# Kernel tuning notes

Measured on AMD Instinct MI355X. Metric: run time of the kernel, lower is better.

Reference implementation:

```python
import jax, jax.numpy as jnp
import numpy as np


def _weighted_sample(key, w, n_draw):
    # Inverse-CDF weighted sampling with replacement; prob proportional to relu(w).
    # Matches torch.multinomial over the strictly-positive (top-cnt sorted) entries,
    # since zero-weight columns are never selected with side='right'.
    cdf = jnp.cumsum(jnp.maximum(w, 0.0), axis=1)                     # [R, C]
    u = jax.random.uniform(key, (w.shape[0], n_draw), dtype=w.dtype) * cdf[:, -1:]
    idx = jax.vmap(lambda c, q: jnp.searchsorted(c, q, side='right'))(cdf, u)
    return jax.lax.stop_gradient(jnp.minimum(idx, w.shape[1] - 1))    # [R, K] column ids


def contrast_loss(key, padj, nadj, px, nx):
    R, Cp = padj.shape
    Cn = nadj.shape[1]
    K = min(Cp, Cn)  # num = min(pcnt, ncnt) <= K always
    pcnt = jnp.sum(padj > 0, axis=1)
    ncnt = jnp.sum(nadj > 0, axis=1)
    num = jnp.minimum(pcnt, ncnt)                                     # [R] int
    pinc = jnp.argsort(padj, axis=1)                                  # ascending, like torch.sort
    ninc = jnp.argsort(nadj, axis=1)
    kp, kn = jax.random.split(key)
    samp_n = _weighted_sample(kn, nadj, K)                            # sampled negative cols
    samp_p = _weighted_sample(kp, padj, K)                            # sampled positive cols
    j = jnp.arange(K)
    mask = (j[None, :] < num[:, None]).astype(px.dtype)               # first num draws count
    rows = jnp.arange(R)[:, None]
    # top-num entries of the ascending sort: positions C-num .. C-1
    top_p = jnp.clip(Cp - num[:, None] + j[None, :], 0, Cp - 1)
    top_n = jnp.clip(Cn - num[:, None] + j[None, :], 0, Cn - 1)
    pos_A = jnp.take_along_axis(pinc, top_p, axis=1)                  # branch num==pcnt
    neg_B = jnp.take_along_axis(ninc, top_n, axis=1)                  # branch num==ncnt<pcnt
    termA = jnp.maximum(nx[rows, samp_n] - px[rows, pos_A] + 1.0, 0.0)
    termB = jnp.maximum(nx[rows, neg_B] - px[rows, samp_p] + 1.0, 0.0)
    branchA = (pcnt <= ncnt)[:, None]                                 # num == pcnt
    term = jnp.where(branchA, termA, termB) * mask
    row_loss = term.sum(axis=1) / jnp.maximum(num, 1).astype(px.dtype)
    return jnp.where(num > 0, row_loss, 0.0).sum()


def _forward(KUU_adj, VUU_adj, Vuser, Vitem, Kuser, Kitem, preference, Vpreference, structure):
    key = jax.random.key(42)
    k0, k1, k2, k3 = jax.random.split(key, 4)
    f32 = VUU_adj.dtype
    # --- Vu: V-user vs V-user ---
    Vu_adj = Vuser @ Vuser.T                                          # [Nv, Nv]
    n = Vu_adj.shape[0]
    tmp1 = 1.0 - (VUU_adj > 0).astype(f32) - jnp.eye(n, dtype=f32)
    Vu = contrast_loss(k0, VUU_adj, tmp1, Vu_adj, Vu_adj)
    # --- Ku: K-user vs K-user (last 3 cols are negatives) ---
    Ku_adj = Kuser @ Kuser.T                                          # [Nk, Nk]
    Kc = KUU_adj.shape[1]
    tmp2 = (1.0 - (KUU_adj > 0).astype(f32) - jnp.eye(Kc, dtype=f32))[:n, -3:]
    Ku = contrast_loss(k1, KUU_adj[:n, :Kc - 3], tmp2,
                       Ku_adj[:n, :Kc - 3], Ku_adj[:n, -3:])
    # --- Vi: V-user vs V-item (binarization of tmp3 is overwritten in the original) ---
    Vi_adj = Vuser @ Vitem.T                                          # [Nv, NvI]
    VUI_adj = Vpreference.T
    Vi = contrast_loss(k2, VUI_adj, 1.0 - VUI_adj, Vi_adj, Vi_adj)
    # --- Ki: first 5 K-users vs K-item ---
    Ki_adj = Kuser[:5, :] @ Kitem.T                                   # [5, NkI]
    KUI_adj = preference.T
    Ki = contrast_loss(k3, KUI_adj, 1.0 - KUI_adj, Ki_adj, Ki_adj)
    # --- ii: item-item structure alignment ---
    ii_adj = Kitem @ Vitem.T                                          # [NkI, NvI]
    ii = jnp.abs(ii_adj - structure[:, :ii_adj.shape[1]]).mean()
    return (Vu, Ku, Vi, Ki, ii)


def setup_inputs() -> dict:
    key = jax.random.key(0)
    ks = jax.random.split(key, 10)
    Nv, Nk, NvI, NkI, d = 2048, 2051, 4096, 4096, 64
    return {
        'KUU_adj': jax.random.normal(ks[0], (Nk, Nk), jnp.float32),
        'VUU_adj': jax.random.normal(ks[1], (Nv, Nv), jnp.float32),
        'Vuser': jax.random.normal(ks[2], (Nv, d), jnp.float32),
        'Vitem': jax.random.normal(ks[3], (NvI, d), jnp.float32),
        'Kuser': jax.random.normal(ks[4], (Nk, d), jnp.float32),
        'Kitem': jax.random.normal(ks[5], (NkI, d), jnp.float32),
        'Vid': jax.random.randint(ks[6], (Nv,), 0, NvI, jnp.int64 if jax.config.jax_enable_x64 else jnp.int32),
        'preference': jax.random.uniform(ks[7], (NkI, 5), jnp.float32),
        'Vpreference': jax.random.uniform(ks[8], (NvI, Nv), jnp.float32),
        'structure': jax.random.normal(ks[9], (NkI, NvI), jnp.float32),
    }


def reference(KUU_adj, VUU_adj, Vuser, Vitem, Kuser, Kitem, Vid, preference, Vpreference, structure):
    # Vid is accepted by the original forward but never used.
    return _forward(KUU_adj, VUU_adj, Vuser, Vitem, Kuser, Kitem, preference, Vpreference, structure)
```

## Files before the change

### kernel.cpp

```cpp
#include <hip/hip_runtime.h>
#include <cstdint>
#include <cstddef>

typedef __attribute__((ext_vector_type(8))) short short8;
typedef __attribute__((ext_vector_type(4))) float f32x4;

__host__ __device__ inline void tf2x32(uint32_t k0, uint32_t k1,
                                       uint32_t c0, uint32_t c1,
                                       uint32_t* o0, uint32_t* o1) {
  uint32_t ks0 = k0, ks1 = k1, ks2 = k0 ^ k1 ^ 0x1BD11BDAu;
  uint32_t x0 = c0 + ks0, x1 = c1 + ks1;
#define TFR(r) { x0 += x1; x1 = (x1 << (r)) | (x1 >> (32 - (r))); x1 ^= x0; }
  TFR(13) TFR(15) TFR(26) TFR(6)   x0 += ks1; x1 += ks2 + 1u;
  TFR(17) TFR(29) TFR(16) TFR(24)  x0 += ks2; x1 += ks0 + 2u;
  TFR(13) TFR(15) TFR(26) TFR(6)   x0 += ks0; x1 += ks1 + 3u;
  TFR(17) TFR(29) TFR(16) TFR(24)  x0 += ks1; x1 += ks2 + 4u;
  TFR(13) TFR(15) TFR(26) TFR(6)   x0 += ks2; x1 += ks0 + 5u;
#undef TFR
  *o0 = x0; *o1 = x1;
}

__device__ inline float tf_u01(uint32_t k0, uint32_t k1, uint32_t c0, uint32_t c1) {
  uint32_t a, b; tf2x32(k0, k1, c0, c1, &a, &b);
  uint32_t bits = a ^ b;
  return __uint_as_float((bits >> 9) | 0x3f800000u) - 1.0f;
}

__device__ inline float mur_u01(uint32_t z, uint32_t salt) {
  z ^= salt;
  z ^= z >> 16; z *= 0x85ebca6bu;
  z ^= z >> 13; z *= 0xc2b2ae35u;
  z ^= z >> 16;
  return __uint_as_float((z >> 9) | 0x3f800000u) - 1.0f;
}

__device__ inline int bsearch_right(const float* cdf, int C, float u) {
  int lo = 0, hi = C;
  while (lo < hi) { int mid = (lo + hi) >> 1; if (cdf[mid] <= u) lo = mid + 1; else hi = mid; }
  return lo < C ? lo : C - 1;
}

__device__ inline uint32_t bfpack(float x, float y) {
  uint32_t a = __float_as_uint(x), b = __float_as_uint(y);
  a = (a + 0x7fffu + ((a >> 16) & 1u)) >> 16;
  b = (b + 0x7fffu + ((b >> 16) & 1u)) >> 16;
  return a | (b << 16);
}

__global__ void init_out(float* out) {
  if (threadIdx.x < 5) out[threadIdx.x] = 0.0f;
}

__global__ void transpose_k(const float* __restrict__ in, float* __restrict__ out,
                            int R, int C) {
  __shared__ float tile[32][33];
  int bx = blockIdx.x * 32;
  int by = blockIdx.y * 32;
  int tx = threadIdx.x, ty = threadIdx.y;
#pragma unroll
  for (int q = 0; q < 32; q += 8)
    tile[ty + q][tx] = in[(size_t)(by + ty + q) * C + (bx + tx)];
  __syncthreads();
#pragma unroll
  for (int q = 0; q < 32; q += 8)
    out[(size_t)(bx + ty + q) * R + (by + tx)] = tile[tx][ty + q];
}

__global__ __launch_bounds__(256) void gemm_nt(
    const float* __restrict__ Arows, const float* __restrict__ Brows,
    float* __restrict__ X, int N) {
  __shared__ __align__(16) float At[64 * 68];
  __shared__ __align__(16) float Bt[64 * 68];
  const int t = threadIdx.x;
  const int i0 = blockIdx.x * 64, j0 = blockIdx.y * 64;
  for (int idx = t; idx < 1024; idx += 256) {
    int row = idx >> 4, q = idx & 15;
    float4 va = *(const float4*)(Arows + (size_t)(i0 + row) * 64 + 4 * q);
    At[(4 * q + 0) * 68 + row] = va.x; At[(4 * q + 1) * 68 + row] = va.y;
    At[(4 * q + 2) * 68 + row] = va.z; At[(4 * q + 3) * 68 + row] = va.w;
    float4 vb = *(const float4*)(Brows + (size_t)(j0 + row) * 64 + 4 * q);
    Bt[(4 * q + 0) * 68 + row] = vb.x; Bt[(4 * q + 1) * 68 + row] = vb.y;
    Bt[(4 * q + 2) * 68 + row] = vb.z; Bt[(4 * q + 3) * 68 + row] = vb.w;
  }
  __syncthreads();
  const int ti = t >> 4, tj = t & 15;
  float acc[4][4] = {{0.f,0.f,0.f,0.f},{0.f,0.f,0.f,0.f},{0.f,0.f,0.f,0.f},{0.f,0.f,0.f,0.f}};
  for (int k = 0; k < 64; ++k) {
    const float4 a = *(const float4*)&At[k * 68 + 4 * ti];
    const float4 b = *(const float4*)&Bt[k * 68 + 4 * tj];
    const float av[4] = {a.x, a.y, a.z, a.w};
    const float bv[4] = {b.x, b.y, b.z, b.w};
#pragma unroll
    for (int p = 0; p < 4; ++p)
#pragma unroll
      for (int q2 = 0; q2 < 4; ++q2) acc[p][q2] += av[p] * bv[q2];
  }
#pragma unroll
  for (int p = 0; p < 4; ++p) {
    float4 w = make_float4(acc[p][0], acc[p][1], acc[p][2], acc[p][3]);
    *(float4*)(X + (size_t)(i0 + 4 * ti + p) * N + j0 + 4 * tj) = w;
  }
}

__global__ __launch_bounds__(256) void ii_mfma(
    const float* __restrict__ Kitem, const float* __restrict__ Vitem,
    const float* __restrict__ structure_, float* __restrict__ out) {
  __shared__ __align__(16) uint32_t Ab[8 * 260];
  __shared__ __align__(16) uint32_t Bb[8 * 260];
  __shared__ float red[256];
  const int t = threadIdx.x;
  const int i0 = blockIdx.x * 64, j0 = blockIdx.y * 64;

  {
    const int m = t >> 2, cq = t & 3;
    const int kk = cq >> 1;
    const int q0 = (cq & 1) * 2;
    const int R = (m >> 4) * 2 + kk;
    const int m15 = m & 15;
    const float4* sa = (const float4*)(Kitem + (size_t)(i0 + m) * 64 + cq * 16);
    const float4* sb = (const float4*)(Vitem + (size_t)(j0 + m) * 64 + cq * 16);
    float4 a0 = sa[0], a1 = sa[1], a2 = sa[2], a3 = sa[3];
    float4 b0 = sb[0], b1 = sb[1], b2 = sb[2], b3 = sb[3];
    uint4 ca0 = make_uint4(bfpack(a0.x, a0.y), bfpack(a0.z, a0.w),
                           bfpack(a1.x, a1.y), bfpack(a1.z, a1.w));
    uint4 ca1 = make_uint4(bfpack(a2.x, a2.y), bfpack(a2.z, a2.w),
                           bfpack(a3.x, a3.y), bfpack(a3.z, a3.w));
    uint4 cb0 = make_uint4(bfpack(b0.x, b0.y), bfpack(b0.z, b0.w),
                           bfpack(b1.x, b1.y), bfpack(b1.z, b1.w));
    uint4 cb1 = make_uint4(bfpack(b2.x, b2.y), bfpack(b2.z, b2.w),
                           bfpack(b3.x, b3.y), bfpack(b3.z, b3.w));
    const int o0 = R * 260 + (((q0 + 0) << 4) | m15) * 4;
    const int o1 = R * 260 + (((q0 + 1) << 4) | m15) * 4;
    *(uint4*)(Ab + o0) = ca0;  *(uint4*)(Ab + o1) = ca1;
    *(uint4*)(Bb + o0) = cb0;  *(uint4*)(Bb + o1) = cb1;
  }
  __syncthreads();

  const int w = t >> 6, l = t & 63;
  short8 afr0 = *(const short8*)(Ab + (w * 2 + 0) * 260 + l * 4);
  short8 afr1 = *(const short8*)(Ab + (w * 2 + 1) * 260 + l * 4);
  f32x4 acc[4];
#pragma unroll
  for (int ct = 0; ct < 4; ++ct) {
    short8 bfr0 = *(const short8*)(Bb + (ct * 2 + 0) * 260 + l * 4);
    short8 bfr1 = *(const short8*)(Bb + (ct * 2 + 1) * 260 + l * 4);
    f32x4 a = {0.0f, 0.0f, 0.0f, 0.0f};
    a = __builtin_amdgcn_mfma_f32_16x16x32_bf16(afr0, bfr0, a, 0, 0, 0);
    a = __builtin_amdgcn_mfma_f32_16x16x32_bf16(afr1, bfr1, a, 0, 0, 0);
    acc[ct] = a;
  }

  const int col = l & 15, rquad = l >> 4;
  float s = 0.0f;
#pragma unroll
  for (int ct = 0; ct < 4; ++ct) {
    const int gc = j0 + ct * 16 + col;
#pragma unroll
    for (int reg = 0; reg < 4; ++reg) {
      const int gr = i0 + w * 16 + rquad * 4 + reg;
      s += fabsf(acc[ct][reg] - structure_[(size_t)gr * 4096 + gc]);
    }
  }
  red[t] = s; __syncthreads();
  for (int off = 128; off > 0; off >>= 1) {
    if (t < off) red[t] += red[t + off];
    __syncthreads();
  }
  if (t == 0) atomicAdd(out + 4, red[0] * (1.0f / 16777216.0f));
}

template <int C, int MODE, bool PRE>
__global__ __launch_bounds__(256) void contrast2(
    const float* __restrict__ padj_mat, size_t rs, size_t cs,
    const float* __restrict__ xmat,
    const float* __restrict__ A, const float* __restrict__ B,
    float* __restrict__ out, int out_idx, uint32_t salt) {
  constexpr int E = C / 256;
  constexpr int LOG2E = (E == 16) ? 4 : 3;
  constexpr int S = (E == 16) ? 260 : 264;
  constexpr int TSZ = (E - 1) * S + 256;
  constexpr int DEPTH = (C == 4096) ? 13 : 12;
  constexpr int NB = 512;
  __shared__ float T[TSZ];
  __shared__ int bs[NB + 1];
  __shared__ float x[PRE ? 1 : C];
  __shared__ __align__(16) float qa[PRE ? 4 : 64];
  __shared__ float red[256];
  __shared__ float wsumsh[4];
  __shared__ int s_pcnt, s_ncnt;
  const int t = threadIdx.x;
  const int r = blockIdx.x;
  const int lane = t & 63, wid = t >> 6;
  const float* xrow = PRE ? (xmat + (size_t)r * C) : nullptr;
  if (t == 0) { s_pcnt = 0; s_ncnt = 0; }
  if (!PRE && t < 64) qa[t] = A[(size_t)r * 64 + t];

  int lp = 0, ln = 0;
  for (int c = t; c < C; c += 256) {
    float v = padj_mat[(size_t)r * rs + (size_t)c * cs];
    T[(c & (E - 1)) * S + (c >> LOG2E)] = v;
    lp += (v > 0.0f) ? 1 : 0;
    if (MODE == 0) ln += (v <= 0.0f && c != r) ? 1 : 0;
    else           ln += ((1.0f - v) > 0.0f) ? 1 : 0;
  }
  if (lp) atomicAdd(&s_pcnt, lp);
  if (ln) atomicAdd(&s_ncnt, ln);
  __syncthreads();

  if (!PRE) {
    const int g = t >> 2, q = t & 3;
    const float4* qa4 = (const float4*)qa;
    for (int c = g; c < C; c += 64) {
      const float4* b4 = (const float4*)(B + (size_t)c * 64);
      float acc = 0.0f;
#pragma unroll
      for (int m = 0; m < 4; ++m) {
        float4 f = b4[q + 4 * m];
        float4 a = qa4[q + 4 * m];
        acc += f.x * a.x + f.y * a.y + f.z * a.z + f.w * a.w;
      }
      acc += __shfl_xor(acc, 1);
      acc += __shfl_xor(acc, 2);
      if (q == 0) x[c] = acc;
    }
    __syncthreads();
  }

  const int pcnt = s_pcnt, ncnt = s_ncnt;
  const int num = min(pcnt, ncnt);
  if (num == 0) return;
  const bool brA = (pcnt <= ncnt);

  auto wf = [&](float v, int c) -> float {
    if (brA) {
      if (MODE == 0) return (v <= 0.0f && c != r) ? 1.0f : 0.0f;
      float nv = 1.0f - v; return nv > 0.0f ? nv : 0.0f;
    }
    return v > 0.0f ? v : 0.0f;
  };

  float csum = 0.0f;
#pragma unroll
  for (int e = 0; e < E; ++e) csum += wf(T[e * S + t], t * E + e);
  float ps = csum;
#pragma unroll
  for (int off = 1; off < 64; off <<= 1) {
    float o = __shfl_up(ps, off);
    if (lane >= off) ps += o;
  }
  if (lane == 63) wsumsh[wid] = ps;
  __syncthreads();
  float wbase = 0.0f;
  for (int w = 0; w < wid; ++w) wbase += wsumsh[w];
  float run = wbase + ps - csum;
  {
#pragma unroll
    for (int e = 0; e < E; ++e) {
      float w = wf(T[e * S + t], t * E + e);
      run += w;
      T[e * S + t] = run;
    }
  }
  __syncthreads();
  const float total = T[(E - 1) * S + 255];

  for (int i = t; i < NB; i += 256) {
    float ub = ((float)i / (float)NB) * total;
    int lo = 0, hi = C;
    for (int it = 0; it < DEPTH; ++it) {
      if (lo < hi) {
        int mid = (lo + hi) >> 1;
        float cv = T[(mid & (E - 1)) * S + (mid >> LOG2E)];
        if (cv <= ub) lo = mid + 1; else hi = mid;
      }
    }
    bs[i] = lo;
  }
  if (t == 0) bs[NB] = C;
  __syncthreads();

  float acc = 0.0f;
  for (int k = 0; k < E; k += 8) {
    int cj[8]; bool dj[8]; float uj[8]; int lo[8], hi[8]; float xc[8];
#pragma unroll
    for (int j = 0; j < 8; ++j) {
      int c = t + (k + j) * 256;
      cj[j] = c;
      float v = padj_mat[(size_t)r * rs + (size_t)c * cs];
      bool det = brA ? (v > 0.0f)
                     : (MODE == 0 ? (v <= 0.0f && c != r) : ((1.0f - v) > 0.0f));
      dj[j] = det;
      xc[j] = PRE ? xrow[c] : x[c];
      float f = mur_u01((uint32_t)(r * C + c), salt);
      uj[j] = f * total;
      int b = (int)(f * (float)NB);
      b = b < NB - 1 ? b : NB - 1; b = b > 0 ? b : 0;
      lo[j] = bs[b]; hi[j] = bs[b + 1];
    }
    for (int it = 0; it < 7; ++it) {
#pragma unroll
      for (int j = 0; j < 8; ++j) {
        int mid = (lo[j] + hi[j]) >> 1;
        float cv = T[(mid & (E - 1)) * S + (mid >> LOG2E)];
        if (lo[j] < hi[j]) {
          if (cv <= uj[j]) lo[j] = mid + 1; else hi[j] = mid;
        }
      }
    }
#pragma unroll
    for (int j = 0; j < 8; ++j) {
      if (dj[j]) {
        int s = lo[j] < C ? lo[j] : C - 1;
        float xs = PRE ? xrow[s] : x[s];
        float term = brA ? (xs - xc[j] + 1.0f) : (xc[j] - xs + 1.0f);
        acc += fmaxf(term, 0.0f);
      }
    }
  }
  red[t] = acc; __syncthreads();
  for (int off = 128; off > 0; off >>= 1) {
    if (t < off) red[t] += red[t + off];
    __syncthreads();
  }
  if (t == 0) atomicAdd(out + out_idx, red[0] / (float)num);
}

__global__ __launch_bounds__(256) void ku_kernel(
    const float* __restrict__ KUU, const float* __restrict__ Kuser,
    float* __restrict__ out,
    uint32_t kp0, uint32_t kp1, uint32_t kn0, uint32_t kn1) {
  const int C = 2048;
  constexpr int E = 8, LOG2E = 3, S = 264;
  constexpr int TSZ = (E - 1) * S + 256;
  __shared__ float T[TSZ];
  __shared__ float red[256];
  __shared__ int s_pcnt;
  const int t = threadIdx.x, r = blockIdx.x;
  const float* row = KUU + (size_t)r * 2051;
  if (t == 0) s_pcnt = 0;
  __syncthreads();
  int lp = 0;
  for (int c = t; c < C; c += 256) {
    float v = row[c];
    T[(c & (E - 1)) * S + (c >> LOG2E)] = v > 0.0f ? v : 0.0f;
    lp += (v > 0.0f) ? 1 : 0;
  }
  if (lp) atomicAdd(&s_pcnt, lp);
  __syncthreads();
  const int pcnt = s_pcnt;
  const float n0 = row[2048], n1 = row[2049], n2 = row[2050];
  const int ng0 = (n0 <= 0.0f), ng1 = (n1 <= 0.0f), ng2 = (n2 <= 0.0f);
  const int ncnt = ng0 + ng1 + ng2;
  const int num = min(pcnt, ncnt);
  if (num == 0) return;

  float csum = 0.0f;
#pragma unroll
  for (int e = 0; e < E; ++e) csum += T[e * S + t];
  red[t] = csum; __syncthreads();
  if (t == 0) {
    float run = 0.0f;
    for (int i = 0; i < 256; ++i) { float v = red[i]; red[i] = run; run += v; }
  }
  __syncthreads();
  {
    float run = red[t];
#pragma unroll
    for (int e = 0; e < E; ++e) { run += T[e * S + t]; T[e * S + t] = run; }
  }
  __syncthreads();
  const float total = T[(E - 1) * S + 255];

  if (pcnt > ncnt) {
    float term = 0.0f;
    if (t < num) {
      int ng[3] = {ng0, ng1, ng2};
      int det = -1, cnt = 0;
      for (int q = 0; q < 3; ++q) {
        if (ng[q]) { if (cnt == t) { det = q; break; } cnt++; }
      }
      float f = tf_u01(kp0, kp1, 0u, (uint32_t)(r * 3 + t));
      float u = f * total;
      int lo = 0, hi = C;
      while (lo < hi) {
        int mid = (lo + hi) >> 1;
        float cv = T[(mid & (E - 1)) * S + (mid >> LOG2E)];
        if (cv <= u) lo = mid + 1; else hi = mid;
      }
      int s = lo < C ? lo : C - 1;
      const float* qr = Kuser + (size_t)r * 64;
      const float* qs = Kuser + (size_t)s * 64;
      const float* qn = Kuser + (size_t)(2048 + det) * 64;
      float px = 0.0f, nx = 0.0f;
      for (int k = 0; k < 64; ++k) { float av = qr[k]; px += av * qs[k]; nx += av * qn[k]; }
      term = fmaxf(nx - px + 1.0f, 0.0f);
    }
    red[t] = term; __syncthreads();
    for (int off = 128; off > 0; off >>= 1) {
      if (t < off) red[t] += red[t + off];
      __syncthreads();
    }
    if (t == 0) atomicAdd(out + 1, red[0] / (float)num);
  } else {
    if (t == 0) {
      float pv[3]; int pi[3]; int np = 0;
      for (int c = 0; c < C; ++c) {
        float v = row[c];
        if (v > 0.0f) { if (np < 3) { pv[np] = v; pi[np] = c; } np++; }
      }
      for (int a2 = 1; a2 < np; ++a2) {
        float v = pv[a2]; int id = pi[a2]; int b2 = a2 - 1;
        while (b2 >= 0 && pv[b2] > v) { pv[b2 + 1] = pv[b2]; pi[b2 + 1] = pi[b2]; b2--; }
        pv[b2 + 1] = v; pi[b2 + 1] = id;
      }
      int ng[3] = {ng0, ng1, ng2};
      float ncdf[3]; float runn = 0.0f;
      for (int q = 0; q < 3; ++q) { runn += ng[q] ? 1.0f : 0.0f; ncdf[q] = runn; }
      float ss = 0.0f;
      for (int j = 0; j < num; ++j) {
        float f = tf_u01(kn0, kn1, 0u, (uint32_t)(r * 3 + j));
        float u = f * runn;
        int s = 0; while (s < 3 && ncdf[s] <= u) s++; if (s > 2) s = 2;
        int det = pi[np - num + j];
        const float* qr = Kuser + (size_t)r * 64;
        const float* qd = Kuser + (size_t)det * 64;
        const float* qn = Kuser + (size_t)(2048 + s) * 64;
        float px = 0.0f, nx = 0.0f;
        for (int k = 0; k < 64; ++k) { float av = qr[k]; px += av * qd[k]; nx += av * qn[k]; }
        ss += fmaxf(nx - px + 1.0f, 0.0f);
      }
      atomicAdd(out + 1, ss / (float)num);
    }
  }
}

__global__ __launch_bounds__(256) void ki_prep(
    const float* __restrict__ preference,
    float* __restrict__ cdf_ws, float* __restrict__ vals_ws,
    int* __restrict__ rank_ws, float* __restrict__ meta) {
  const int C = 4096;
  __shared__ float cdf[4096];
  __shared__ float red[256];
  __shared__ int s_pcnt;
  const int t = threadIdx.x, r = blockIdx.x;
  if (t == 0) s_pcnt = 0;
  __syncthreads();
  for (int i = r * 256 + t; i < 5 * C; i += 5 * 256) rank_ws[i] = 0;
  int lp = 0;
  for (int c = t; c < C; c += 256) {
    float v = preference[(size_t)c * 5 + r];
    lp += (v > 0.0f) ? 1 : 0;
    cdf[c] = 1.0f - v;
    vals_ws[(size_t)r * C + c] = v;
  }
  if (lp) atomicAdd(&s_pcnt, lp);
  __syncthreads();
  const int num = s_pcnt;
  const int E = C >> 8;
  const int base = t * E;
  float csum = 0.0f;
  for (int e = 0; e < E; ++e) csum += cdf[base + e];
  red[t] = csum; __syncthreads();
  if (t == 0) {
    float run = 0.0f;
    for (int i = 0; i < 256; ++i) { float v = red[i]; red[i] = run; run += v; }
  }
  __syncthreads();
  {
    float run = red[t];
    for (int e = 0; e < E; ++e) { float w = cdf[base + e]; run += w; cdf[base + e] = run; }
  }
  __syncthreads();
  for (int c = t; c < C; c += 256) cdf_ws[(size_t)r * C + c] = cdf[c];
  if (t == 0) { meta[2 * r] = (float)num; meta[2 * r + 1] = cdf[C - 1]; }
}

__global__ __launch_bounds__(256) void ki_rank_p(
    const float* __restrict__ vals_ws, int* __restrict__ rank_ws) {
  const int C = 4096;
  __shared__ __align__(16) float sv[256];
  const int t = threadIdx.x;
  const int r = blockIdx.y;
  const int z = blockIdx.z;
  const int c0 = blockIdx.x * 256 + t;
  const float* vrow = vals_ws + (size_t)r * C;
  sv[t] = vrow[z * 256 + t];
  __syncthreads();
  const float v0 = vrow[c0];
  const int cbase = z * 256;
  int rank = 0;
  const float4* sv4 = (const float4*)sv;
#pragma unroll 8
  for (int q = 0; q < 64; ++q) {
    float4 w = sv4[q];
    int cb = cbase + 4 * q;
    rank += (w.x < v0 || (w.x == v0 && cb + 0 < c0)) ? 1 : 0;
    rank += (w.y < v0 || (w.y == v0 && cb + 1 < c0)) ? 1 : 0;
    rank += (w.z < v0 || (w.z == v0 && cb + 2 < c0)) ? 1 : 0;
    rank += (w.w < v0 || (w.w == v0 && cb + 3 < c0)) ? 1 : 0;
  }
  if (rank) atomicAdd(&rank_ws[(size_t)r * C + c0], rank);
}

__global__ __launch_bounds__(256) void ki_scatter(
    const int* __restrict__ rank_ws, int* __restrict__ sorted_ws) {
  const int C = 4096;
  const int t = threadIdx.x;
  const int r = blockIdx.y;
  const int c0 = blockIdx.x * 256 + t;
  sorted_ws[(size_t)r * C + rank_ws[(size_t)r * C + c0]] = c0;
}

__global__ __launch_bounds__(256) void ki_draw(
    const float* __restrict__ cdf_ws, const int* __restrict__ sorted_ws,
    const float* __restrict__ meta,
    const float* __restrict__ Kuser, const float* __restrict__ Kitem,
    float* __restrict__ out, uint32_t kn0, uint32_t kn1) {
  const int C = 4096;
  __shared__ float cdf[4096];
  __shared__ __align__(16) float qa[64];
  __shared__ float red[256];
  const int t = threadIdx.x;
  const int r = blockIdx.y;
  const int j = blockIdx.x * 256 + t;
  if (t < 64) qa[t] = Kuser[(size_t)r * 64 + t];
  for (int c = t; c < C; c += 256) cdf[c] = cdf_ws[(size_t)r * C + c];
  __syncthreads();
  const int num = (int)meta[2 * r];
  const float total = meta[2 * r + 1];
  float acc = 0.0f;
  if (j < num) {
    float f = tf_u01(kn0, kn1, 0u, (uint32_t)(r * 4096 + j));
    float u = f * total;
    int s = bsearch_right(cdf, C, u);
    int det = sorted_ws[(size_t)r * C + (C - num + j)];
    const float4* qa4 = (const float4*)qa;
    const float4* bs = (const float4*)(Kitem + (size_t)s * 64);
    const float4* bd = (const float4*)(Kitem + (size_t)det * 64);
    float xs = 0.0f, xd = 0.0f;
#pragma unroll
    for (int m = 0; m < 16; ++m) {
      float4 a4 = qa4[m]; float4 v1 = bs[m]; float4 v2 = bd[m];
      xs += a4.x * v1.x + a4.y * v1.y + a4.z * v1.z + a4.w * v1.w;
      xd += a4.x * v2.x + a4.y * v2.y + a4.z * v2.z + a4.w * v2.w;
    }
    acc = fmaxf(xs - xd + 1.0f, 0.0f) / (float)num;
  }
  red[t] = acc; __syncthreads();
  for (int off = 128; off > 0; off >>= 1) {
    if (t < off) red[t] += red[t + off];
    __syncthreads();
  }
  if (t == 0 && red[0] != 0.0f) atomicAdd(out + 3, red[0]);
}

__global__ __launch_bounds__(256) void ki_kernel(
    const float* __restrict__ preference, const float* __restrict__ Kuser,
    const float* __restrict__ Kitem, float* __restrict__ out,
    uint32_t kn0, uint32_t kn1) {
  const int C = 4096;
  __shared__ float cdf[4096];
  __shared__ unsigned long long skey[4096];
  __shared__ __align__(16) float qa[64];
  __shared__ float red[256];
  __shared__ int s_pcnt;
  const int t = threadIdx.x, r = blockIdx.x;
  if (t == 0) s_pcnt = 0;
  if (t < 64) qa[t] = Kuser[(size_t)r * 64 + t];
  __syncthreads();
  int lp = 0;
  for (int c = t; c < C; c += 256) {
    float v = preference[(size_t)c * 5 + r];
    lp += (v > 0.0f) ? 1 : 0;
    cdf[c] = 1.0f - v;
    skey[c] = ((unsigned long long)__float_as_uint(v) << 32) | (unsigned)c;
  }
  if (lp) atomicAdd(&s_pcnt, lp);
  __syncthreads();
  const int num = s_pcnt;
  if (num == 0) return;
  const int E = C >> 8;
  const int base = t * E;
  float csum = 0.0f;
  for (int e = 0; e < E; ++e) csum += cdf[base + e];
  red[t] = csum; __syncthreads();
  if (t == 0) {
    float run = 0.0f;
    for (int i = 0; i < 256; ++i) { float v = red[i]; red[i] = run; run += v; }
  }
  __syncthreads();
  {
    float run = red[t];
    for (int e = 0; e < E; ++e) { float w = cdf[base + e]; run += w; cdf[base + e] = run; }
  }
  __syncthreads();
  const float total = cdf[C - 1];
  for (int k = 2; k <= C; k <<= 1) {
    for (int j2 = k >> 1; j2 > 0; j2 >>= 1) {
      for (int i = t; i < C; i += 256) {
        int ixj = i ^ j2;
        if (ixj > i) {
          unsigned long long a = skey[i], b = skey[ixj];
          bool up = ((i & k) == 0);
          if ((a > b) == up) { skey[i] = b; skey[ixj] = a; }
        }
      }
      __syncthreads();
    }
  }
  float acc = 0.0f;
  const float4* qa4 = (const float4*)qa;
  for (int j = t; j < num; j += 256) {
    float f = tf_u01(kn0, kn1, 0u, (uint32_t)(r * 4096 + j));
    float u = f * total;
    int s = bsearch_right(cdf, C, u);
    int det = (int)(skey[C - num + j] & 0xffffffffull);
    const float4* bs = (const float4*)(Kitem + (size_t)s * 64);
    const float4* bd = (const float4*)(Kitem + (size_t)det * 64);
    float xs = 0.0f, xd = 0.0f;
#pragma unroll
    for (int m = 0; m < 16; ++m) {
      float4 a4 = qa4[m]; float4 v1 = bs[m]; float4 v2 = bd[m];
      xs += a4.x * v1.x + a4.y * v1.y + a4.z * v1.z + a4.w * v1.w;
      xd += a4.x * v2.x + a4.y * v2.y + a4.z * v2.z + a4.w * v2.w;
    }
    acc += fmaxf(xs - xd + 1.0f, 0.0f);
  }
  red[t] = acc; __syncthreads();
  for (int off = 128; off > 0; off >>= 1) {
    if (t < off) red[t] += red[t + off];
    __syncthreads();
  }
  if (t == 0) atomicAdd(out + 3, red[0] / (float)num);
}

extern "C" void kernel_launch(void* const* d_in, const int* in_sizes, int n_in,
                              void* d_out, int out_size, void* d_ws, size_t ws_size,
                              hipStream_t stream) {
  const float* KUU   = (const float*)d_in[0];
  const float* VUU   = (const float*)d_in[1];
  const float* Vuser = (const float*)d_in[2];
  const float* Vitem = (const float*)d_in[3];
  const float* Kuser = (const float*)d_in[4];
  const float* Kitem = (const float*)d_in[5];
  const float* pref  = (const float*)d_in[7];
  const float* Vpref = (const float*)d_in[8];
  const float* structure_ = (const float*)d_in[9];
  float* out = (float*)d_out;

  uint32_t k1a, k1b, k3a, k3b;
  tf2x32(0u, 42u, 0u, 1u, &k1a, &k1b);
  tf2x32(0u, 42u, 0u, 3u, &k3a, &k3b);
  uint32_t kup0, kup1, kun0, kun1, kin0, kin1;
  tf2x32(k1a, k1b, 0u, 0u, &kup0, &kup1);
  tf2x32(k1a, k1b, 0u, 1u, &kun0, &kun1);
  tf2x32(k3a, k3b, 0u, 1u, &kin0, &kin1);

  const uint32_t SALT_VU = 0x8AF1B0C2u;
  const uint32_t SALT_VI = 0x5F356495u;

  const size_t vuit_bytes = (size_t)2048 * 4096 * sizeof(float);
  const size_t xvi_bytes  = (size_t)2048 * 4096 * sizeof(float);
  const size_t xvu_bytes  = (size_t)2048 * 2048 * sizeof(float);
  const size_t ki_bytes   = (size_t)(4 * 5 * 4096 + 16) * sizeof(float);
  const size_t full_bytes = vuit_bytes + xvi_bytes + xvu_bytes + ki_bytes;

  const bool full = ws_size >= full_bytes;
  const bool mid  = !full && ws_size >= vuit_bytes + ki_bytes;

  hipLaunchKernelGGL(init_out, dim3(1), dim3(64), 0, stream, out);

  if (full) {
    float* VUIt = (float*)d_ws;
    float* Xvi  = (float*)((char*)d_ws + vuit_bytes);
    float* Xvu  = (float*)((char*)d_ws + vuit_bytes + xvi_bytes);
    char*  kib  = (char*)d_ws + vuit_bytes + xvi_bytes + xvu_bytes;
    float* cdf_ws  = (float*)kib;
    float* vals_ws = cdf_ws + 5 * 4096;
    int*   sorted_ws = (int*)(vals_ws + 5 * 4096);
    int*   rank_ws = sorted_ws + 5 * 4096;
    float* meta = (float*)(rank_ws + 5 * 4096);

    hipLaunchKernelGGL(ki_prep, dim3(5), dim3(256), 0, stream,
                       pref, cdf_ws, vals_ws, rank_ws, meta);
    hipLaunchKernelGGL(ki_rank_p, dim3(16, 5, 16), dim3(256), 0, stream,
                       vals_ws, rank_ws);
    hipLaunchKernelGGL(ki_scatter, dim3(16, 5), dim3(256), 0, stream,
                       rank_ws, sorted_ws);
    hipLaunchKernelGGL(ki_draw, dim3(16, 5), dim3(256), 0, stream,
                       cdf_ws, sorted_ws, meta, Kuser, Kitem, out, kin0, kin1);

    hipLaunchKernelGGL(transpose_k, dim3(64, 128), dim3(32, 8), 0, stream,
                       Vpref, VUIt, 4096, 2048);
    hipLaunchKernelGGL(gemm_nt, dim3(32, 32), dim3(256), 0, stream,
                       Vuser, Vuser, Xvu, 2048);
    hipLaunchKernelGGL(gemm_nt, dim3(32, 64), dim3(256), 0, stream,
                       Vuser, Vitem, Xvi, 4096);
    hipLaunchKernelGGL(ii_mfma, dim3(64, 64), dim3(256), 0, stream,
                       Kitem, Vitem, structure_, out);

    hipLaunchKernelGGL((contrast2<2048, 0, true>), dim3(2048), dim3(256), 0, stream,
                       VUU, (size_t)2048, (size_t)1, Xvu, nullptr, nullptr,
                       out, 0, SALT_VU);
    hipLaunchKernelGGL(ku_kernel, dim3(2048), dim3(256), 0, stream,
                       KUU, Kuser, out, kup0, kup1, kun0, kun1);
    hipLaunchKernelGGL((contrast2<4096, 1, true>), dim3(2048), dim3(256), 0, stream,
                       VUIt, (size_t)4096, (size_t)1, Xvi, nullptr, nullptr,
                       out, 2, SALT_VI);
  } else if (mid) {
    float* VUIt = (float*)d_ws;
    char*  kib  = (char*)d_ws + vuit_bytes;
    float* cdf_ws  = (float*)kib;
    float* vals_ws = cdf_ws + 5 * 4096;
    int*   sorted_ws = (int*)(vals_ws + 5 * 4096);
    int*   rank_ws = sorted_ws + 5 * 4096;
    float* meta = (float*)(rank_ws + 5 * 4096);

    hipLaunchKernelGGL(ki_prep, dim3(5), dim3(256), 0, stream,
                       pref, cdf_ws, vals_ws, rank_ws, meta);
    hipLaunchKernelGGL(ki_rank_p, dim3(16, 5, 16), dim3(256), 0, stream,
                       vals_ws, rank_ws);
    hipLaunchKernelGGL(ki_scatter, dim3(16, 5), dim3(256), 0, stream,
                       rank_ws, sorted_ws);
    hipLaunchKernelGGL(ki_draw, dim3(16, 5), dim3(256), 0, stream,
                       cdf_ws, sorted_ws, meta, Kuser, Kitem, out, kin0, kin1);

    hipLaunchKernelGGL(ii_mfma, dim3(64, 64), dim3(256), 0, stream,
                       Kitem, Vitem, structure_, out);
    hipLaunchKernelGGL(transpose_k, dim3(64, 128), dim3(32, 8), 0, stream,
                       Vpref, VUIt, 4096, 2048);
    hipLaunchKernelGGL((contrast2<2048, 0, false>), dim3(2048), dim3(256), 0, stream,
                       VUU, (size_t)2048, (size_t)1, nullptr, Vuser, Vuser,
                       out, 0, SALT_VU);
    hipLaunchKernelGGL(ku_kernel, dim3(2048), dim3(256), 0, stream,
                       KUU, Kuser, out, kup0, kup1, kun0, kun1);
    hipLaunchKernelGGL((contrast2<4096, 1, false>), dim3(2048), dim3(256), 0, stream,
                       VUIt, (size_t)4096, (size_t)1, nullptr, Vuser, Vitem,
                       out, 2, SALT_VI);
  } else {
    hipLaunchKernelGGL(ii_mfma, dim3(64, 64), dim3(256), 0, stream,
                       Kitem, Vitem, structure_, out);
    hipLaunchKernelGGL((contrast2<2048, 0, false>), dim3(2048), dim3(256), 0, stream,
                       VUU, (size_t)2048, (size_t)1, nullptr, Vuser, Vuser,
                       out, 0, SALT_VU);
    hipLaunchKernelGGL(ku_kernel, dim3(2048), dim3(256), 0, stream,
                       KUU, Kuser, out, kup0, kup1, kun0, kun1);
    hipLaunchKernelGGL((contrast2<4096, 1, false>), dim3(2048), dim3(256), 0, stream,
                       Vpref, (size_t)1, (size_t)2048, nullptr, Vuser, Vitem,
                       out, 2, SALT_VI);
    hipLaunchKernelGGL(ki_kernel, dim3(5), dim3(256), 0, stream,
                       pref, Kuser, Kitem, out, kin0, kin1);
  }
}
```

Baseline: 417.3 us.

## Replace scalar atomics with per-block partial buffers and a final reduction kernel

```diff
diff --git a/kernel.cpp b/kernel.cpp
--- a/kernel.cpp
+++ b/kernel.cpp
@@ -47,8 +47,41 @@
   return a | (b << 16);
 }
 
+#define PART_VU 0
+#define PART_KU 2048
+#define PART_VI 4096
+#define PART_KI 6144
+#define PART_II 6224
+#define PART_LEN 10320
+
 __global__ void init_out(float* out) {
   if (threadIdx.x < 5) out[threadIdx.x] = 0.0f;
+}
+
+__global__ void zero_part(float* part) {
+  for (int i = blockIdx.x * 256 + threadIdx.x; i < PART_LEN; i += gridDim.x * 256)
+    part[i] = 0.0f;
+}
+
+__global__ __launch_bounds__(256) void final_reduce(
+    const float* __restrict__ part, float* __restrict__ out) {
+  __shared__ float red[256];
+  const int t = threadIdx.x;
+  const int idx = blockIdx.x;
+  int off, len; float scale = 1.0f;
+  if (idx == 0)      { off = PART_VU; len = 2048; }
+  else if (idx == 1) { off = PART_KU; len = 2048; }
+  else if (idx == 2) { off = PART_VI; len = 2048; }
+  else if (idx == 3) { off = PART_KI; len = 80;   }
+  else               { off = PART_II; len = 4096; scale = 1.0f / 16777216.0f; }
+  float s = 0.0f;
+  for (int i = t; i < len; i += 256) s += part[off + i];
+  red[t] = s; __syncthreads();
+  for (int o = 128; o > 0; o >>= 1) {
+    if (t < o) red[t] += red[t + o];
+    __syncthreads();
+  }
+  if (t == 0) out[idx] = red[0] * scale;
 }
 
 __global__ void transpose_k(const float* __restrict__ in, float* __restrict__ out,
@@ -104,10 +137,13 @@
 
 __global__ __launch_bounds__(256) void ii_mfma(
     const float* __restrict__ Kitem, const float* __restrict__ Vitem,
-    const float* __restrict__ structure_, float* __restrict__ out) {
-  __shared__ __align__(16) uint32_t Ab[8 * 260];
-  __shared__ __align__(16) uint32_t Bb[8 * 260];
+    const float* __restrict__ structure_, float* __restrict__ out,
+    float* __restrict__ part) {
+  __shared__ __align__(16) uint32_t smem[4352];
   __shared__ float red[256];
+  uint32_t* Ab = smem;
+  uint32_t* Bb = smem + 2080;
+  float* Dsh = (float*)smem;
   const int t = threadIdx.x;
   const int i0 = blockIdx.x * 64, j0 = blockIdx.y * 64;
 
@@ -149,24 +185,36 @@
     a = __builtin_amdgcn_mfma_f32_16x16x32_bf16(afr1, bfr1, a, 0, 0, 0);
     acc[ct] = a;
   }
+  __syncthreads();
 
   const int col = l & 15, rquad = l >> 4;
+#pragma unroll
+  for (int ct = 0; ct < 4; ++ct)
+#pragma unroll
+    for (int reg = 0; reg < 4; ++reg)
+      Dsh[(w * 16 + rquad * 4 + reg) * 68 + ct * 16 + col] = acc[ct][reg];
+  __syncthreads();
+
+  const int row = t >> 2, c0q = (t & 3) * 16;
+  const float4* srow = (const float4*)(structure_ + (size_t)(i0 + row) * 4096 + j0 + c0q);
+  const float4* drow = (const float4*)(Dsh + row * 68 + c0q);
   float s = 0.0f;
 #pragma unroll
-  for (int ct = 0; ct < 4; ++ct) {
-    const int gc = j0 + ct * 16 + col;
-#pragma unroll
-    for (int reg = 0; reg < 4; ++reg) {
-      const int gr = i0 + w * 16 + rquad * 4 + reg;
-      s += fabsf(acc[ct][reg] - structure_[(size_t)gr * 4096 + gc]);
-    }
+  for (int q = 0; q < 4; ++q) {
+    float4 sv = srow[q];
+    float4 dv = drow[q];
+    s += fabsf(dv.x - sv.x) + fabsf(dv.y - sv.y)
+       + fabsf(dv.z - sv.z) + fabsf(dv.w - sv.w);
   }
   red[t] = s; __syncthreads();
   for (int off = 128; off > 0; off >>= 1) {
     if (t < off) red[t] += red[t + off];
     __syncthreads();
   }
-  if (t == 0) atomicAdd(out + 4, red[0] * (1.0f / 16777216.0f));
+  if (t == 0) {
+    if (part) part[blockIdx.y * gridDim.x + blockIdx.x] = red[0];
+    else atomicAdd(out + 4, red[0] * (1.0f / 16777216.0f));
+  }
 }
 
 template <int C, int MODE, bool PRE>
@@ -174,7 +222,8 @@
     const float* __restrict__ padj_mat, size_t rs, size_t cs,
     const float* __restrict__ xmat,
     const float* __restrict__ A, const float* __restrict__ B,
-    float* __restrict__ out, int out_idx, uint32_t salt) {
+    float* __restrict__ out, int out_idx, uint32_t salt,
+    float* __restrict__ part) {
   constexpr int E = C / 256;
   constexpr int LOG2E = (E == 16) ? 4 : 3;
   constexpr int S = (E == 16) ? 260 : 264;
@@ -322,13 +371,17 @@
     if (t < off) red[t] += red[t + off];
     __syncthreads();
   }
-  if (t == 0) atomicAdd(out + out_idx, red[0] / (float)num);
+  if (t == 0) {
+    if (part) part[r] = red[0] / (float)num;
+    else atomicAdd(out + out_idx, red[0] / (float)num);
+  }
 }
 
 __global__ __launch_bounds__(256) void ku_kernel(
     const float* __restrict__ KUU, const float* __restrict__ Kuser,
     float* __restrict__ out,
-    uint32_t kp0, uint32_t kp1, uint32_t kn0, uint32_t kn1) {
+    uint32_t kp0, uint32_t kp1, uint32_t kn0, uint32_t kn1,
+    float* __restrict__ part) {
   const int C = 2048;
   constexpr int E = 8, LOG2E = 3, S = 264;
   constexpr int TSZ = (E - 1) * S + 256;
@@ -400,7 +453,10 @@
       if (t < off) red[t] += red[t + off];
       __syncthreads();
     }
-    if (t == 0) atomicAdd(out + 1, red[0] / (float)num);
+    if (t == 0) {
+      if (part) part[r] = red[0] / (float)num;
+      else atomicAdd(out + 1, red[0] / (float)num);
+    }
   } else {
     if (t == 0) {
       float pv[3]; int pi[3]; int np = 0;
@@ -429,7 +485,8 @@
         for (int k = 0; k < 64; ++k) { float av = qr[k]; px += av * qd[k]; nx += av * qn[k]; }
         ss += fmaxf(nx - px + 1.0f, 0.0f);
       }
-      atomicAdd(out + 1, ss / (float)num);
+      if (part) part[r] = ss / (float)num;
+      else atomicAdd(out + 1, ss / (float)num);
     }
   }
 }
@@ -515,7 +572,8 @@
     const float* __restrict__ cdf_ws, const int* __restrict__ sorted_ws,
     const float* __restrict__ meta,
     const float* __restrict__ Kuser, const float* __restrict__ Kitem,
-    float* __restrict__ out, uint32_t kn0, uint32_t kn1) {
+    float* __restrict__ out, uint32_t kn0, uint32_t kn1,
+    float* __restrict__ part) {
   const int C = 4096;
   __shared__ float cdf[4096];
   __shared__ __align__(16) float qa[64];
@@ -535,12 +593,12 @@
     int s = bsearch_right(cdf, C, u);
     int det = sorted_ws[(size_t)r * C + (C - num + j)];
     const float4* qa4 = (const float4*)qa;
-    const float4* bs = (const float4*)(Kitem + (size_t)s * 64);
-    const float4* bd = (const float4*)(Kitem + (size_t)det * 64);
+    const float4* bsv = (const float4*)(Kitem + (size_t)s * 64);
+    const float4* bdv = (const float4*)(Kitem + (size_t)det * 64);
     float xs = 0.0f, xd = 0.0f;
 #pragma unroll
     for (int m = 0; m < 16; ++m) {
-      float4 a4 = qa4[m]; float4 v1 = bs[m]; float4 v2 = bd[m];
+      float4 a4 = qa4[m]; float4 v1 = bsv[m]; float4 v2 = bdv[m];
       xs += a4.x * v1.x + a4.y * v1.y + a4.z * v1.z + a4.w * v1.w;
       xd += a4.x * v2.x + a4.y * v2.y + a4.z * v2.z + a4.w * v2.w;
     }
@@ -551,7 +609,10 @@
     if (t < off) red[t] += red[t + off];
     __syncthreads();
   }
-  if (t == 0 && red[0] != 0.0f) atomicAdd(out + 3, red[0]);
+  if (t == 0) {
+    if (part) part[r * 16 + blockIdx.x] = red[0];
+    else if (red[0] != 0.0f) atomicAdd(out + 3, red[0]);
+  }
 }
 
 __global__ __launch_bounds__(256) void ki_kernel(
@@ -615,12 +676,12 @@
     float u = f * total;
     int s = bsearch_right(cdf, C, u);
     int det = (int)(skey[C - num + j] & 0xffffffffull);
-    const float4* bs = (const float4*)(Kitem + (size_t)s * 64);
-    const float4* bd = (const float4*)(Kitem + (size_t)det * 64);
+    const float4* bsv = (const float4*)(Kitem + (size_t)s * 64);
+    const float4* bdv = (const float4*)(Kitem + (size_t)det * 64);
     float xs = 0.0f, xd = 0.0f;
 #pragma unroll
     for (int m = 0; m < 16; ++m) {
-      float4 a4 = qa4[m]; float4 v1 = bs[m]; float4 v2 = bd[m];
+      float4 a4 = qa4[m]; float4 v1 = bsv[m]; float4 v2 = bdv[m];
       xs += a4.x * v1.x + a4.y * v1.y + a4.z * v1.z + a4.w * v1.w;
       xd += a4.x * v2.x + a4.y * v2.y + a4.z * v2.z + a4.w * v2.w;
     }
@@ -663,23 +724,25 @@
   const size_t xvi_bytes  = (size_t)2048 * 4096 * sizeof(float);
   const size_t xvu_bytes  = (size_t)2048 * 2048 * sizeof(float);
   const size_t ki_bytes   = (size_t)(4 * 5 * 4096 + 16) * sizeof(float);
-  const size_t full_bytes = vuit_bytes + xvi_bytes + xvu_bytes + ki_bytes;
+  const size_t part_bytes = (size_t)PART_LEN * sizeof(float);
+  const size_t full_bytes = vuit_bytes + xvi_bytes + xvu_bytes + ki_bytes + part_bytes;
 
   const bool full = ws_size >= full_bytes;
-  const bool mid  = !full && ws_size >= vuit_bytes + ki_bytes;
-
-  hipLaunchKernelGGL(init_out, dim3(1), dim3(64), 0, stream, out);
-
-  if (full) {
+  const bool mid  = !full && ws_size >= vuit_bytes + ki_bytes + part_bytes;
+
+  if (full || mid) {
     float* VUIt = (float*)d_ws;
-    float* Xvi  = (float*)((char*)d_ws + vuit_bytes);
-    float* Xvu  = (float*)((char*)d_ws + vuit_bytes + xvi_bytes);
-    char*  kib  = (char*)d_ws + vuit_bytes + xvi_bytes + xvu_bytes;
+    float* Xvi  = full ? (float*)((char*)d_ws + vuit_bytes) : nullptr;
+    float* Xvu  = full ? (float*)((char*)d_ws + vuit_bytes + xvi_bytes) : nullptr;
+    char*  kib  = (char*)d_ws + (full ? vuit_bytes + xvi_bytes + xvu_bytes : vuit_bytes);
     float* cdf_ws  = (float*)kib;
     float* vals_ws = cdf_ws + 5 * 4096;
     int*   sorted_ws = (int*)(vals_ws + 5 * 4096);
     int*   rank_ws = sorted_ws + 5 * 4096;
     float* meta = (float*)(rank_ws + 5 * 4096);
+    float* part = meta + 16;
+
+    hipLaunchKernelGGL(zero_part, dim3(16), dim3(256), 0, stream, part);
 
     hipLaunchKernelGGL(ki_prep, dim3(5), dim3(256), 0, stream,
                        pref, cdf_ws, vals_ws, rank_ws, meta);
@@ -688,66 +751,54 @@
     hipLaunchKernelGGL(ki_scatter, dim3(16, 5), dim3(256), 0, stream,
                        rank_ws, sorted_ws);
     hipLaunchKernelGGL(ki_draw, dim3(16, 5), dim3(256), 0, stream,
-                       cdf_ws, sorted_ws, meta, Kuser, Kitem, out, kin0, kin1);
+                       cdf_ws, sorted_ws, meta, Kuser, Kitem, out, kin0, kin1,
+                       part + PART_KI);
 
     hipLaunchKernelGGL(transpose_k, dim3(64, 128), dim3(32, 8), 0, stream,
                        Vpref, VUIt, 4096, 2048);
-    hipLaunchKernelGGL(gemm_nt, dim3(32, 32), dim3(256), 0, stream,
-                       Vuser, Vuser, Xvu, 2048);
-    hipLaunchKernelGGL(gemm_nt, dim3(32, 64), dim3(256), 0, stream,
-                       Vuser, Vitem, Xvi, 4096);
+    if (full) {
+      hipLaunchKernelGGL(gemm_nt, dim3(32, 32), dim3(256), 0, stream,
+                         Vuser, Vuser, Xvu, 2048);
+      hipLaunchKernelGGL(gemm_nt, dim3(32, 64), dim3(256), 0, stream,
+                         Vuser, Vitem, Xvi, 4096);
+    }
     hipLaunchKernelGGL(ii_mfma, dim3(64, 64), dim3(256), 0, stream,
-                       Kitem, Vitem, structure_, out);
-
-    hipLaunchKernelGGL((contrast2<2048, 0, true>), dim3(2048), dim3(256), 0, stream,
-                       VUU, (size_t)2048, (size_t)1, Xvu, nullptr, nullptr,
-                       out, 0, SALT_VU);
+                       Kitem, Vitem, structure_, out, part + PART_II);
+
+    if (full) {
+      hipLaunchKernelGGL((contrast2<2048, 0, true>), dim3(2048), dim3(256), 0, stream,
+                         VUU, (size_t)2048, (size_t)1, Xvu, nullptr, nullptr,
+                         out, 0, SALT_VU, part + PART_VU);
+    } else {
+      hipLaunchKernelGGL((contrast2<2048, 0, false>), dim3(2048), dim3(256), 0, stream,
+                         VUU, (size_t)2048, (size_t)1, nullptr, Vuser, Vuser,
+                         out, 0, SALT_VU, part + PART_VU);
+    }
     hipLaunchKernelGGL(ku_kernel, dim3(2048), dim3(256), 0, stream,
-                       KUU, Kuser, out, kup0, kup1, kun0, kun1);
-    hipLaunchKernelGGL((contrast2<4096, 1, true>), dim3(2048), dim3(256), 0, stream,
-                       VUIt, (size_t)4096, (size_t)1, Xvi, nullptr, nullptr,
-                       out, 2, SALT_VI);
-  } else if (mid) {
-    float* VUIt = (float*)d_ws;
-    char*  kib  = (char*)d_ws + vuit_bytes;
-    float* cdf_ws  = (float*)kib;
-    float* vals_ws = cdf_ws + 5 * 4096;
-    int*   sorted_ws = (int*)(vals_ws + 5 * 4096);
-    int*   rank_ws = sorted_ws + 5 * 4096;
-    float* meta = (float*)(rank_ws + 5 * 4096);
-
-    hipLaunchKernelGGL(ki_prep, dim3(5), dim3(256), 0, stream,
-                       pref, cdf_ws, vals_ws, rank_ws, meta);
-    hipLaunchKernelGGL(ki_rank_p, dim3(16, 5, 16), dim3(256), 0, stream,
-                       vals_ws, rank_ws);
-    hipLaunchKernelGGL(ki_scatter, dim3(16, 5), dim3(256), 0, stream,
-                       rank_ws, sorted_ws);
-    hipLaunchKernelGGL(ki_draw, dim3(16, 5), dim3(256), 0, stream,
-                       cdf_ws, sorted_ws, meta, Kuser, Kitem, out, kin0, kin1);
-
+                       KUU, Kuser, out, kup0, kup1, kun0, kun1, part + PART_KU);
+    if (full) {
+      hipLaunchKernelGGL((contrast2<4096, 1, true>), dim3(2048), dim3(256), 0, stream,
+                         VUIt, (size_t)4096, (size_t)1, Xvi, nullptr, nullptr,
+                         out, 2, SALT_VI, part + PART_VI);
+    } else {
+      hipLaunchKernelGGL((contrast2<4096, 1, false>), dim3(2048), dim3(256), 0, stream,
+                         VUIt, (size_t)4096, (size_t)1, nullptr, Vuser, Vitem,
+                         out, 2, SALT_VI, part + PART_VI);
+    }
+
+    hipLaunchKernelGGL(final_reduce, dim3(5), dim3(256), 0, stream, part, out);
+  } else {
+    hipLaunchKernelGGL(init_out, dim3(1), dim3(64), 0, stream, out);
     hipLaunchKernelGGL(ii_mfma, dim3(64, 64), dim3(256), 0, stream,
-                       Kitem, Vitem, structure_, out);
-    hipLaunchKernelGGL(transpose_k, dim3(64, 128), dim3(32, 8), 0, stream,
-                       Vpref, VUIt, 4096, 2048);
+                       Kitem, Vitem, structure_, out, (float*)nullptr);
     hipLaunchKernelGGL((contrast2<2048, 0, false>), dim3(2048), dim3(256), 0, stream,
                        VUU, (size_t)2048, (size_t)1, nullptr, Vuser, Vuser,
-                       out, 0, SALT_VU);
+                       out, 0, SALT_VU, (float*)nullptr);
     hipLaunchKernelGGL(ku_kernel, dim3(2048), dim3(256), 0, stream,
-                       KUU, Kuser, out, kup0, kup1, kun0, kun1);
-    hipLaunchKernelGGL((contrast2<4096, 1, false>), dim3(2048), dim3(256), 0, stream,
-                       VUIt, (size_t)4096, (size_t)1, nullptr, Vuser, Vitem,
-                       out, 2, SALT_VI);
-  } else {
-    hipLaunchKernelGGL(ii_mfma, dim3(64, 64), dim3(256), 0, stream,
-                       Kitem, Vitem, structure_, out);
-    hipLaunchKernelGGL((contrast2<2048, 0, false>), dim3(2048), dim3(256), 0, stream,
-                       VUU, (size_t)2048, (size_t)1, nullptr, Vuser, Vuser,
-                       out, 0, SALT_VU);
-    hipLaunchKernelGGL(ku_kernel, dim3(2048), dim3(256), 0, stream,
-                       KUU, Kuser, out, kup0, kup1, kun0, kun1);
+                       KUU, Kuser, out, kup0, kup1, kun0, kun1, (float*)nullptr);
     hipLaunchKernelGGL((contrast2<4096, 1, false>), dim3(2048), dim3(256), 0, stream,
                        Vpref, (size_t)1, (size_t)2048, nullptr, Vuser, Vitem,
-                       out, 2, SALT_VI);
+                       out, 2, SALT_VI, (float*)nullptr);
     hipLaunchKernelGGL(ki_kernel, dim3(5), dim3(256), 0, stream,
                        pref, Kuser, Kitem, out, kin0, kin1);
   }
```

Measured after the change: 350.0 us. 16.1% less time.
